# Performance work log

Measured on AMD Instinct MI355X. Metric: run time of the kernel, lower is better.

## Reference

```python
import jax, jax.numpy as jnp
import numpy as np

T = 16777216  # series length (2**24)


def setup_inputs() -> dict:
    key = jax.random.key(0)
    k1, k2 = jax.random.split(key)
    timeseries = jax.random.normal(k1, (T,), dtype=jnp.float32)
    # learned smoothing parameter alpha in (0, 1), per min_max_norm(0, 1) constraint
    alpha = jax.random.uniform(k2, (1,), dtype=jnp.float32)
    return {"timeseries": timeseries, "alpha": alpha}


def reference(timeseries, alpha):
    """Simple exponential smoothing (component form).

    level_0 = y_0; level_t = (1-alpha)*level_{t-1} + alpha*y_t for t >= 1.
    prediction_t (the forecast emitted at step t) is the level BEFORE the
    update, so the output is levels[0 : T-1], length T-1 (matches the
    original loop that emits one forecast per timestep in timeseries[1:]).

    Expressed as a first-order linear recurrence s_t = a_t * s_{t-1} + b_t
    and solved with an associative (parallel) scan.
    """
    a0 = alpha[0]
    n = timeseries.shape[0]
    dt = timeseries.dtype
    # a_0 = 0, b_0 = y_0 pins level_0 = y_0 regardless of the dummy carry.
    a = jnp.concatenate([jnp.zeros((1,), dt),
                         jnp.full((n - 1,), 1.0, dt) * (1.0 - a0)])
    b = jnp.concatenate([timeseries[:1], a0 * timeseries[1:]])

    def combine(e1, e2):
        a1, b1 = e1
        a2, b2 = e2
        return (a1 * a2, a2 * b1 + b2)

    _, levels = jax.lax.associative_scan(combine, (a, b))  # levels[t] = level_t
    return levels[:-1]
```

## Files before the change

### kernel.cpp

```cpp
#include <hip/hip_runtime.h>
#include <stdint.h>


#define BLOCK 256
#define SEG   64
#define VPT   (SEG / 4)
#define CHUNK (BLOCK * SEG)
#define ROWS  65
#define HALO  4096
#define HSEG  (HALO / BLOCK)
#define HVPT  (HSEG / 4)
#define DECAY_THR 1e-8f

typedef float f32x4 __attribute__((ext_vector_type(4)));

__device__ __forceinline__ void nt_store4(float* p, float x, float y, float z, float w) {
    f32x4 v = {x, y, z, w};
    __builtin_nontemporal_store(v, (f32x4*)p);
}

__device__ __forceinline__ float pow2k(float x, int k) {
    float p = x;
#pragma unroll
    for (int i = 0; i < k; ++i) p *= p;
    return p;
}

__device__ __forceinline__ void block_scan_affine(float* sa, float* sb, int t) {
#pragma unroll
    for (int off = 1; off < BLOCK; off <<= 1) {
        float pa = 1.0f, pb = 0.0f;
        if (t >= off) { pa = sa[t - off]; pb = sb[t - off]; }
        __syncthreads();
        if (t >= off) {
            float ca = sa[t], cb = sb[t];
            sa[t] = pa * ca;
            sb[t] = fmaf(ca, pb, cb);
        }
        __syncthreads();
    }
}

__global__ __launch_bounds__(BLOCK) void k_block_agg(
    const float* __restrict__ y, const float* __restrict__ alpha_p,
    float* __restrict__ aggA, float* __restrict__ aggB, long n)
{
    const float alpha = alpha_p[0];
    const float oma = 1.0f - alpha;
    if (pow2k(oma, 12) < DECAY_THR) return;

    const int t = threadIdx.x;
    const long base = (long)blockIdx.x * CHUNK + (long)t * SEG;

    float a = 1.0f, s = 0.0f;
    if (base + SEG <= n) {
        const float4* p = (const float4*)(y + base);
#pragma unroll
        for (int v = 0; v < VPT; ++v) {
            float4 q = p[v];
            s = fmaf(oma, s, alpha * q.x);
            s = fmaf(oma, s, alpha * q.y);
            s = fmaf(oma, s, alpha * q.z);
            s = fmaf(oma, s, alpha * q.w);
        }
        a = pow2k(oma, 6);
    } else {
        for (int k = 0; k < SEG; ++k) {
            long idx = base + k;
            if (idx < n) { s = fmaf(oma, s, alpha * y[idx]); a *= oma; }
        }
    }

    __shared__ float sa[BLOCK], sb[BLOCK];
    sa[t] = a; sb[t] = s;
    __syncthreads();
    block_scan_affine(sa, sb, t);
    if (t == BLOCK - 1) {
        aggA[blockIdx.x] = sa[t];
        aggB[blockIdx.x] = sb[t];
    }
}

__global__ __launch_bounds__(BLOCK, 4) void k_emit_fused(
    const float* __restrict__ y, const float* __restrict__ alpha_p,
    const float* __restrict__ aggA, const float* __restrict__ aggB,
    float* __restrict__ out, long n, int G)
{
    __shared__ float sa[BLOCK], sb[BLOCK];
    __shared__ float stage[2 * 64 * ROWS];
    __shared__ float s_carry;

    const int t = threadIdx.x;
    int tile = blockIdx.x;
    if ((G & 7) == 0) tile = (tile & 7) * (G >> 3) + (tile >> 3);

    const float alpha = alpha_p[0];
    const float oma   = 1.0f - alpha;
    const bool  fast  = (pow2k(oma, 12) < DECAY_THR);
    const long tbase = (long)tile * CHUNK;
    const long base  = tbase + (long)t * SEG;
    const bool fullTile = (tbase + CHUNK <= n);
    const float y0 = y[0];

    const bool do_halo = fast && (tile > 0);
    float4 hq[HVPT];
    if (do_halo) {
        const float4* hp = (const float4*)(y + (tbase - HALO)) + t * HVPT;
#pragma unroll
        for (int v = 0; v < HVPT; ++v) hq[v] = hp[v];
    }

    float4 arr[VPT];
    float a_seg, b_seg;
    if (fullTile) {
        const float4* p = (const float4*)(y + base);
#pragma unroll
        for (int v = 0; v < VPT; ++v) arr[v] = p[v];
        float s = 0.0f;
#pragma unroll
        for (int v = 0; v < VPT; ++v) {
            s = fmaf(oma, s, alpha * arr[v].x);
            s = fmaf(oma, s, alpha * arr[v].y);
            s = fmaf(oma, s, alpha * arr[v].z);
            s = fmaf(oma, s, alpha * arr[v].w);
        }
        b_seg = s;
        a_seg = pow2k(oma, 6);
    } else {
        float a = 1.0f, s = 0.0f;
        for (int k = 0; k < SEG; ++k) {
            long idx = base + k;
            if (idx < n) { s = fmaf(oma, s, alpha * y[idx]); a *= oma; }
        }
        a_seg = a; b_seg = s;
    }

    float carry_fast = y0;
    if (do_halo) {
        float hs = 0.0f;
#pragma unroll
        for (int v = 0; v < HVPT; ++v) {
            hs = fmaf(oma, hs, alpha * hq[v].x);
            hs = fmaf(oma, hs, alpha * hq[v].y);
            hs = fmaf(oma, hs, alpha * hq[v].z);
            hs = fmaf(oma, hs, alpha * hq[v].w);
        }
        sa[t] = pow2k(oma, 4);
        sb[t] = hs;
        __syncthreads();
        block_scan_affine(sa, sb, t);
        carry_fast = sb[BLOCK - 1];
        __syncthreads();
    }

    sa[t] = a_seg; sb[t] = b_seg;
    __syncthreads();
    block_scan_affine(sa, sb, t);

    float ea_th = 1.0f, eb_th = 0.0f;
    if (t > 0) { ea_th = sa[t - 1]; eb_th = sb[t - 1]; }

    float carry;
    if (fast) {
        carry = carry_fast;
    } else {
        const int items = (G + BLOCK - 1) / BLOCK;
        float ta = 1.0f, tb = 0.0f;
        for (int j = 0; j < items; ++j) {
            int g = t * items + j;
            if (g < G) {
                float ca = aggA[g], cb = aggB[g];
                tb = fmaf(ca, tb, cb);
                ta *= ca;
            }
        }
        __syncthreads();
        sa[t] = ta; sb[t] = tb;
        __syncthreads();
        block_scan_affine(sa, sb, t);

        const int q = tile / items;
        if (t == q) {
            float ea = (q > 0) ? sa[q - 1] : 1.0f;
            float eb = (q > 0) ? sb[q - 1] : 0.0f;
            const int r = tile - q * items;
            for (int j = 0; j < r; ++j) {
                int g = q * items + j;
                float ca = aggA[g], cb = aggB[g];
                eb = fmaf(ca, eb, cb);
                ea *= ca;
            }
            s_carry = fmaf(ea, y0, eb);
        }
        __syncthreads();
        carry = s_carry;
    }

    float lvl = fmaf(ea_th, carry, eb_th);

    if (fullTile) {
#pragma unroll
        for (int v = 0; v < VPT; ++v) {
            float4 q4 = arr[v], r;
            lvl = fmaf(oma, lvl, alpha * q4.x); r.x = lvl;
            lvl = fmaf(oma, lvl, alpha * q4.y); r.y = lvl;
            lvl = fmaf(oma, lvl, alpha * q4.z); r.z = lvl;
            lvl = fmaf(oma, lvl, alpha * q4.w); r.w = lvl;
            arr[v] = r;
        }
        const int  wv = t >> 6;
        const int  ln = t & 63;
        const bool lastGuard = (tbase + CHUNK > n - 1);
#pragma unroll
        for (int p = 0; p < 2; ++p) {
            __syncthreads();
            if ((wv >> 1) == p) {
                int g = ((wv & 1) << 6) | ln;
                float* row = &stage[g * ROWS];
#pragma unroll
                for (int v = 0; v < VPT; ++v) {
                    row[4 * v + 0] = arr[v].x;
                    row[4 * v + 1] = arr[v].y;
                    row[4 * v + 2] = arr[v].z;
                    row[4 * v + 3] = arr[v].w;
                }
            }
            __syncthreads();
            const long rbase = tbase + (long)p * 8192;
#pragma unroll
            for (int k = 0; k < 8; ++k) {
                int jj = t + (k << 8);
                int g  = jj >> 4;
                int e  = (jj << 2) & 63;
                const float* row = &stage[g * ROWS + e];
                float rx = row[0], ry = row[1], rz = row[2], rw = row[3];
                long gi = rbase + 4 * (long)jj;
                if (!lastGuard) {
                    nt_store4(out + gi, rx, ry, rz, rw);
                } else {
                    if (gi + 4 <= n - 1) {
                        nt_store4(out + gi, rx, ry, rz, rw);
                    } else {
                        if (gi + 0 < n - 1) out[gi + 0] = rx;
                        if (gi + 1 < n - 1) out[gi + 1] = ry;
                        if (gi + 2 < n - 1) out[gi + 2] = rz;
                        if (gi + 3 < n - 1) out[gi + 3] = rw;
                    }
                }
            }
        }
    } else {
        for (int k = 0; k < SEG; ++k) {
            long idx = base + k;
            if (idx < n) {
                lvl = fmaf(oma, lvl, alpha * y[idx]);
                if (idx < n - 1) out[idx] = lvl;
            }
        }
    }
}

extern "C" void kernel_launch(void* const* d_in, const int* in_sizes, int n_in,
                              void* d_out, int out_size, void* d_ws, size_t ws_size,
                              hipStream_t stream) {
    const float* y     = (const float*)d_in[0];
    const float* alpha = (const float*)d_in[1];
    float* out = (float*)d_out;
    const long n = (long)in_sizes[0];
    const int  G = (int)((n + CHUNK - 1) / CHUNK);

    float* aggA = (float*)d_ws;
    float* aggB = aggA + G;

    k_block_agg<<<G, BLOCK, 0, stream>>>(y, alpha, aggA, aggB, n);
    k_emit_fused<<<G, BLOCK, 0, stream>>>(y, alpha, aggA, aggB, out, n, G);
}
```

Baseline: 141.6 us.

## Use wavefront shuffle scans, smaller segments, and drop LDS store staging

Replaces the shared-memory Hillis-Steele block scan with a 64-lane shuffle scan plus a small cross-wave combine, which removes most barriers. It halves the per-thread segment to 32 and drops the register-held input array and the padded LDS transpose used to coalesce output stores, raising the launch-bounds occupancy target. The emit pass now re-reads the input from global memory for the second sweep and writes float4s straight from each thread, using strided rather than fully coalesced writes and normal instead of nontemporal stores. The halo carry path now uses the same wave scan.

```diff
diff --git a/kernel.cpp b/kernel.cpp
--- a/kernel.cpp
+++ b/kernel.cpp
@@ -3,22 +3,14 @@
 
 
 #define BLOCK 256
-#define SEG   64
+#define SEG   32
 #define VPT   (SEG / 4)
 #define CHUNK (BLOCK * SEG)
-#define ROWS  65
 #define HALO  4096
 #define HSEG  (HALO / BLOCK)
 #define HVPT  (HSEG / 4)
 #define DECAY_THR 1e-8f
 
-typedef float f32x4 __attribute__((ext_vector_type(4)));
-
-__device__ __forceinline__ void nt_store4(float* p, float x, float y, float z, float w) {
-    f32x4 v = {x, y, z, w};
-    __builtin_nontemporal_store(v, (f32x4*)p);
-}
-
 __device__ __forceinline__ float pow2k(float x, int k) {
     float p = x;
 #pragma unroll
@@ -26,19 +18,41 @@
     return p;
 }
 
-__device__ __forceinline__ void block_scan_affine(float* sa, float* sb, int t) {
-#pragma unroll
-    for (int off = 1; off < BLOCK; off <<= 1) {
-        float pa = 1.0f, pb = 0.0f;
-        if (t >= off) { pa = sa[t - off]; pb = sb[t - off]; }
-        __syncthreads();
-        if (t >= off) {
-            float ca = sa[t], cb = sb[t];
-            sa[t] = pa * ca;
-            sb[t] = fmaf(ca, pb, cb);
-        }
-        __syncthreads();
-    }
+__device__ __forceinline__ void wave_scan_affine(float& a, float& b) {
+    const int lane = threadIdx.x & 63;
+#pragma unroll
+    for (int off = 1; off < 64; off <<= 1) {
+        float pa = __shfl_up(a, off);
+        float pb = __shfl_up(b, off);
+        if (lane >= off) {
+            b = fmaf(a, pb, b);
+            a = pa * a;
+        }
+    }
+}
+
+__device__ __forceinline__ void block_exscan_affine(
+    float a, float b, float* wa, float* wb, int t, float& ea, float& eb)
+{
+    float ia = a, ib = b;
+    wave_scan_affine(ia, ib);
+    const int w = t >> 6, lane = t & 63;
+    if (lane == 63) { wa[w] = ia; wb[w] = ib; }
+    float xa = __shfl_up(ia, 1);
+    float xb = __shfl_up(ib, 1);
+    if (lane == 0) { xa = 1.0f; xb = 0.0f; }
+    __syncthreads();
+    float pa = 1.0f, pb = 0.0f;
+#pragma unroll
+    for (int i = 0; i < 3; ++i) {
+        if (i < w) {
+            float ca = wa[i], cb = wb[i];
+            pb = fmaf(ca, pb, cb);
+            pa *= ca;
+        }
+    }
+    eb = fmaf(xa, pb, xb);
+    ea = pa * xa;
 }
 
 __global__ __launch_bounds__(BLOCK) void k_block_agg(
@@ -63,7 +77,7 @@
             s = fmaf(oma, s, alpha * q.z);
             s = fmaf(oma, s, alpha * q.w);
         }
-        a = pow2k(oma, 6);
+        a = pow2k(oma, 5);
     } else {
         for (int k = 0; k < SEG; ++k) {
             long idx = base + k;
@@ -71,23 +85,29 @@
         }
     }
 
-    __shared__ float sa[BLOCK], sb[BLOCK];
-    sa[t] = a; sb[t] = s;
+    __shared__ float wa[4], wb[4];
+    wave_scan_affine(a, s);
+    if ((t & 63) == 63) { wa[t >> 6] = a; wb[t >> 6] = s; }
     __syncthreads();
-    block_scan_affine(sa, sb, t);
-    if (t == BLOCK - 1) {
-        aggA[blockIdx.x] = sa[t];
-        aggB[blockIdx.x] = sb[t];
-    }
-}
-
-__global__ __launch_bounds__(BLOCK, 4) void k_emit_fused(
+    if (t == 0) {
+        float ta = 1.0f, tb = 0.0f;
+#pragma unroll
+        for (int i = 0; i < 4; ++i) {
+            float ca = wa[i], cb = wb[i];
+            tb = fmaf(ca, tb, cb);
+            ta *= ca;
+        }
+        aggA[blockIdx.x] = ta;
+        aggB[blockIdx.x] = tb;
+    }
+}
+
+__global__ __launch_bounds__(BLOCK, 8) void k_emit(
     const float* __restrict__ y, const float* __restrict__ alpha_p,
     const float* __restrict__ aggA, const float* __restrict__ aggB,
     float* __restrict__ out, long n, int G)
 {
-    __shared__ float sa[BLOCK], sb[BLOCK];
-    __shared__ float stage[2 * 64 * ROWS];
+    __shared__ float wa[4], wb[4];
     __shared__ float s_carry;
 
     const int t = threadIdx.x;
@@ -102,30 +122,20 @@
     const bool fullTile = (tbase + CHUNK <= n);
     const float y0 = y[0];
 
-    const bool do_halo = fast && (tile > 0);
-    float4 hq[HVPT];
-    if (do_halo) {
-        const float4* hp = (const float4*)(y + (tbase - HALO)) + t * HVPT;
-#pragma unroll
-        for (int v = 0; v < HVPT; ++v) hq[v] = hp[v];
-    }
-
-    float4 arr[VPT];
     float a_seg, b_seg;
     if (fullTile) {
         const float4* p = (const float4*)(y + base);
-#pragma unroll
-        for (int v = 0; v < VPT; ++v) arr[v] = p[v];
         float s = 0.0f;
 #pragma unroll
         for (int v = 0; v < VPT; ++v) {
-            s = fmaf(oma, s, alpha * arr[v].x);
-            s = fmaf(oma, s, alpha * arr[v].y);
-            s = fmaf(oma, s, alpha * arr[v].z);
-            s = fmaf(oma, s, alpha * arr[v].w);
+            float4 q = p[v];
+            s = fmaf(oma, s, alpha * q.x);
+            s = fmaf(oma, s, alpha * q.y);
+            s = fmaf(oma, s, alpha * q.z);
+            s = fmaf(oma, s, alpha * q.w);
         }
         b_seg = s;
-        a_seg = pow2k(oma, 6);
+        a_seg = pow2k(oma, 5);
     } else {
         float a = 1.0f, s = 0.0f;
         for (int k = 0; k < SEG; ++k) {
@@ -135,35 +145,37 @@
         a_seg = a; b_seg = s;
     }
 
-    float carry_fast = y0;
-    if (do_halo) {
-        float hs = 0.0f;
-#pragma unroll
-        for (int v = 0; v < HVPT; ++v) {
-            hs = fmaf(oma, hs, alpha * hq[v].x);
-            hs = fmaf(oma, hs, alpha * hq[v].y);
-            hs = fmaf(oma, hs, alpha * hq[v].z);
-            hs = fmaf(oma, hs, alpha * hq[v].w);
-        }
-        sa[t] = pow2k(oma, 4);
-        sb[t] = hs;
-        __syncthreads();
-        block_scan_affine(sa, sb, t);
-        carry_fast = sb[BLOCK - 1];
-        __syncthreads();
-    }
-
-    sa[t] = a_seg; sb[t] = b_seg;
-    __syncthreads();
-    block_scan_affine(sa, sb, t);
-
-    float ea_th = 1.0f, eb_th = 0.0f;
-    if (t > 0) { ea_th = sa[t - 1]; eb_th = sb[t - 1]; }
-
-    float carry;
+    float carry = y0;
     if (fast) {
-        carry = carry_fast;
-    } else {
+        if (tile > 0) {
+            const float4* hp = (const float4*)(y + (tbase - HALO)) + t * HVPT;
+            float hs = 0.0f;
+#pragma unroll
+            for (int v = 0; v < HVPT; ++v) {
+                float4 q = hp[v];
+                hs = fmaf(oma, hs, alpha * q.x);
+                hs = fmaf(oma, hs, alpha * q.y);
+                hs = fmaf(oma, hs, alpha * q.z);
+                hs = fmaf(oma, hs, alpha * q.w);
+            }
+            float ha = pow2k(oma, 4);
+            wave_scan_affine(ha, hs);
+            if ((t & 63) == 63) { wa[t >> 6] = ha; wb[t >> 6] = hs; }
+            __syncthreads();
+            float cb_ = 0.0f;
+#pragma unroll
+            for (int i = 0; i < 4; ++i) {
+                cb_ = fmaf(wa[i], cb_, wb[i]);
+            }
+            carry = cb_;
+            __syncthreads();
+        }
+    }
+
+    float ea_th, eb_th;
+    block_exscan_affine(a_seg, b_seg, wa, wb, t, ea_th, eb_th);
+
+    if (!fast) {
         const int items = (G + BLOCK - 1) / BLOCK;
         float ta = 1.0f, tb = 0.0f;
         for (int j = 0; j < items; ++j) {
@@ -175,14 +187,11 @@
             }
         }
         __syncthreads();
-        sa[t] = ta; sb[t] = tb;
-        __syncthreads();
-        block_scan_affine(sa, sb, t);
-
+        float pa, pb;
+        block_exscan_affine(ta, tb, wa, wb, t, pa, pb);
         const int q = tile / items;
         if (t == q) {
-            float ea = (q > 0) ? sa[q - 1] : 1.0f;
-            float eb = (q > 0) ? sb[q - 1] : 0.0f;
+            float ea = pa, eb = pb;
             const int r = tile - q * items;
             for (int j = 0; j < r; ++j) {
                 int g = q * items + j;
@@ -199,53 +208,26 @@
     float lvl = fmaf(ea_th, carry, eb_th);
 
     if (fullTile) {
+        const float4* p = (const float4*)(y + base);
+        const bool guard = (base + SEG > n - 1);
 #pragma unroll
         for (int v = 0; v < VPT; ++v) {
-            float4 q4 = arr[v], r;
-            lvl = fmaf(oma, lvl, alpha * q4.x); r.x = lvl;
-            lvl = fmaf(oma, lvl, alpha * q4.y); r.y = lvl;
-            lvl = fmaf(oma, lvl, alpha * q4.z); r.z = lvl;
-            lvl = fmaf(oma, lvl, alpha * q4.w); r.w = lvl;
-            arr[v] = r;
-        }
-        const int  wv = t >> 6;
-        const int  ln = t & 63;
-        const bool lastGuard = (tbase + CHUNK > n - 1);
-#pragma unroll
-        for (int p = 0; p < 2; ++p) {
-            __syncthreads();
-            if ((wv >> 1) == p) {
-                int g = ((wv & 1) << 6) | ln;
-                float* row = &stage[g * ROWS];
-#pragma unroll
-                for (int v = 0; v < VPT; ++v) {
-                    row[4 * v + 0] = arr[v].x;
-                    row[4 * v + 1] = arr[v].y;
-                    row[4 * v + 2] = arr[v].z;
-                    row[4 * v + 3] = arr[v].w;
-                }
-            }
-            __syncthreads();
-            const long rbase = tbase + (long)p * 8192;
-#pragma unroll
-            for (int k = 0; k < 8; ++k) {
-                int jj = t + (k << 8);
-                int g  = jj >> 4;
-                int e  = (jj << 2) & 63;
-                const float* row = &stage[g * ROWS + e];
-                float rx = row[0], ry = row[1], rz = row[2], rw = row[3];
-                long gi = rbase + 4 * (long)jj;
-                if (!lastGuard) {
-                    nt_store4(out + gi, rx, ry, rz, rw);
+            float4 q = p[v], r;
+            lvl = fmaf(oma, lvl, alpha * q.x); r.x = lvl;
+            lvl = fmaf(oma, lvl, alpha * q.y); r.y = lvl;
+            lvl = fmaf(oma, lvl, alpha * q.z); r.z = lvl;
+            lvl = fmaf(oma, lvl, alpha * q.w); r.w = lvl;
+            const long gi = base + 4 * (long)v;
+            if (!guard) {
+                *(float4*)(out + gi) = r;
+            } else {
+                if (gi + 4 <= n - 1) {
+                    *(float4*)(out + gi) = r;
                 } else {
-                    if (gi + 4 <= n - 1) {
-                        nt_store4(out + gi, rx, ry, rz, rw);
-                    } else {
-                        if (gi + 0 < n - 1) out[gi + 0] = rx;
-                        if (gi + 1 < n - 1) out[gi + 1] = ry;
-                        if (gi + 2 < n - 1) out[gi + 2] = rz;
-                        if (gi + 3 < n - 1) out[gi + 3] = rw;
-                    }
+                    if (gi + 0 < n - 1) out[gi + 0] = r.x;
+                    if (gi + 1 < n - 1) out[gi + 1] = r.y;
+                    if (gi + 2 < n - 1) out[gi + 2] = r.z;
+                    if (gi + 3 < n - 1) out[gi + 3] = r.w;
                 }
             }
         }
@@ -273,5 +255,5 @@
     float* aggB = aggA + G;
 
     k_block_agg<<<G, BLOCK, 0, stream>>>(y, alpha, aggA, aggB, n);
-    k_emit_fused<<<G, BLOCK, 0, stream>>>(y, alpha, aggA, aggB, out, n, G);
-}
+    k_emit<<<G, BLOCK, 0, stream>>>(y, alpha, aggA, aggB, out, n, G);
+}
```

New measurement: 199.7 us. 41.0% more time.
